# Kernel tuning notes

Hardware: AMD Instinct MI355X
Metric: run time of the kernel (lower is better)

The kernel has to match this reference:

```python
import jax, jax.numpy as jnp
import numpy as np

B, S, D = 2, 2048, 1024
H, HD = 16, 64

def setup_inputs() -> dict:
    key = jax.random.key(0)
    k1, k2, k3, k4 = jax.random.split(key, 4)
    inputs = jax.random.normal(k1, (B, S, D), dtype=jnp.float32)
    scale = 1.0 / np.sqrt(D)
    Wq = jax.random.normal(k2, (D, H * HD), dtype=jnp.float32) * scale
    Wk = jax.random.normal(k3, (D, H * HD), dtype=jnp.float32) * scale
    Wv = jax.random.normal(k4, (D, H * HD), dtype=jnp.float32) * scale
    return {"inputs": inputs, "Wq": Wq, "Wk": Wk, "Wv": Wv}

def _split_heads(x):
    # [B,S,H*HD] -> [B,H,S,HD]; tf.split along last axis == reshape then transpose
    b, s, _ = x.shape
    return x.reshape(b, s, H, HD).transpose(0, 2, 1, 3)

def reference(inputs, Wq, Wk, Wv):
    q = _split_heads(inputs @ Wq)  # [B,H,S,HD]
    k = _split_heads(inputs @ Wk)
    v = _split_heads(inputs @ Wv)
    scores = jnp.einsum("bhsd,bhtd->bhst", q, k) / jnp.sqrt(jnp.float32(HD))
    attn = jax.nn.softmax(scores, axis=-1)  # [B,H,S,S]
    out = jnp.einsum("bhst,bhtd->bhsd", attn, v)  # [B,H,S,HD]
    # concat heads back: [B,S,H*HD]
    return out.transpose(0, 2, 1, 3).reshape(inputs.shape[0], inputs.shape[1], H * HD)
```

## Files before the change

### kernel.cpp

```cpp
#include <hip/hip_runtime.h>
#include <hip/hip_fp16.h>

typedef __attribute__((ext_vector_type(8))) short short8;
typedef __attribute__((ext_vector_type(4))) float f32x4;
typedef __attribute__((ext_vector_type(16))) float f32x16;

#define B_  2
#define S_  2048
#define D_  1024
#define H_  16
#define HD_ 64
#define M_  (B_*S_)
#define N_  (H_*HD_)
#define HSZ ((size_t)B_*H_*S_*HD_)
#define BHS_ (B_*H_*S_)

#define QSCALE 0.18033688011112042f
#define M0 8.0f

__device__ __forceinline__ unsigned short f2bf(float f) {
  unsigned int u = __float_as_uint(f);
  u += 0x7fffu + ((u >> 16) & 1u);
  return (unsigned short)(u >> 16);
}

__device__ __forceinline__ unsigned int cvt_pk_bf16(float lo, float hi) {
  unsigned int r;
  asm("v_cvt_pk_bf16_f32 %0, %1, %2" : "=v"(r) : "v"(lo), "v"(hi));
  return r;
}

__device__ __forceinline__ float exp2_fast(float x) {
  float r;
  asm("v_exp_f32 %0, %1" : "=v"(r) : "v"(x));
  return r;
}

__device__ __forceinline__ void gll16(const void* g, void* l) {
  __builtin_amdgcn_global_load_lds(
      (const __attribute__((address_space(1))) void*)g,
      (__attribute__((address_space(3))) void*)l, 16, 0, 0);
}

__global__ __launch_bounds__(256) void cvt_all_kernel(const float* __restrict__ x,
                                                      const float* __restrict__ w0,
                                                      const float* __restrict__ w1,
                                                      const float* __restrict__ w2,
                                                      unsigned short* __restrict__ xb,
                                                      unsigned short* __restrict__ wt) {
  __shared__ float tile[32][33];
  int bid = blockIdx.x;
  if (bid < 4096) {
    int i = bid * 256 + threadIdx.x;
    float4 v = reinterpret_cast<const float4*>(x)[i];
    ushort4 o;
    o.x = f2bf(v.x); o.y = f2bf(v.y); o.z = f2bf(v.z); o.w = f2bf(v.w);
    reinterpret_cast<ushort4*>(xb)[i] = o;
    return;
  }
  int wid = bid - 4096;
  int z = wid >> 10, rem = wid & 1023;
  int nbase = (rem & 31) * 32, kbase = (rem >> 5) * 32;
  int tx = threadIdx.x & 31, ty = threadIdx.x >> 5;
  const float* w = z == 0 ? w0 : (z == 1 ? w1 : w2);
  unsigned short* o = wt + (size_t)z * D_ * N_;
#pragma unroll
  for (int i = 0; i < 4; i++)
    tile[ty + i*8][tx] = w[(size_t)(kbase + ty + i*8) * N_ + nbase + tx];
  __syncthreads();
#pragma unroll
  for (int i = 0; i < 4; i++)
    o[(size_t)(nbase + ty + i*8) * D_ + kbase + tx] = f2bf(tile[tx][ty + i*8]);
}

__global__ __launch_bounds__(256) void qkv_gemm_kernel(const unsigned short* __restrict__ xbp,
                                                       const unsigned short* __restrict__ wt,
                                                       unsigned short* __restrict__ qkv) {
  __shared__ __align__(16) unsigned short As[2][128 * 64];
  __shared__ __align__(16) unsigned short Bs[2][128 * 64];
  int hid = blockIdx.x;
  int wq = (hid & 7) * 96 + (hid >> 3);
  int z = wq >> 8, gy = (wq >> 3) & 31, gx = wq & 7;
  const unsigned short* w = wt + (size_t)z * D_ * N_;
  unsigned short* out = qkv + (size_t)z * HSZ;
  int lane = threadIdx.x & 63, wave = threadIdx.x >> 6;
  int lr = lane & 15, lk = lane >> 4;
  int mblk = gy * 128, nblk = gx * 128;
  int wm = (wave >> 1) * 64, wn = (wave & 1) * 64;

  int srow0 = wave * 32 + (lane >> 3);
  int scol = lane & 7;
  f32x4 acc[4][4] = {};

#define STAGE_G(b, kk) do {                                                      \
    _Pragma("unroll")                                                            \
    for (int it = 0; it < 4; it++) {                                             \
      int row = srow0 + it * 8;                                                  \
      int ce = (scol ^ (row & 7)) * 8;                                           \
      gll16(xbp + (size_t)(mblk + row) * D_ + (kk) + ce,                         \
            (void*)(As[b] + (size_t)(wave * 4 + it) * 512));                     \
      gll16(w   + (size_t)(nblk + row) * D_ + (kk) + ce,                         \
            (void*)(Bs[b] + (size_t)(wave * 4 + it) * 512));                     \
    }                                                                            \
  } while (0)

  STAGE_G(0, 0);

  for (int kt = 0; kt < 16; kt++) {
    int bufg = kt & 1;
    __syncthreads();
    if (kt < 15) STAGE_G(bufg ^ 1, (kt + 1) * 64);

    short8 a[2][4], b[2][4];
#pragma unroll
    for (int i = 0; i < 4; i++) {
      int row = wm + i * 16 + lr;
      const char* rp = (const char*)As[bufg] + row * 128;
#pragma unroll
      for (int ks = 0; ks < 2; ks++)
        a[ks][i] = *reinterpret_cast<const short8*>(rp + ((((ks*4 + lk) ^ (row & 7))) << 4));
    }
#pragma unroll
    for (int j = 0; j < 4; j++) {
      int row = wn + j * 16 + lr;
      const char* rp = (const char*)Bs[bufg] + row * 128;
#pragma unroll
      for (int ks = 0; ks < 2; ks++)
        b[ks][j] = *reinterpret_cast<const short8*>(rp + ((((ks*4 + lk) ^ (row & 7))) << 4));
    }
    if (z == 2) {
#pragma unroll
      for (int ks = 0; ks < 2; ks++)
#pragma unroll
        for (int i = 0; i < 4; i++)
#pragma unroll
          for (int j = 0; j < 4; j++)
            acc[i][j] = __builtin_amdgcn_mfma_f32_16x16x32_bf16(a[ks][i], b[ks][j], acc[i][j], 0, 0, 0);
    } else {
#pragma unroll
      for (int ks = 0; ks < 2; ks++)
#pragma unroll
        for (int i = 0; i < 4; i++)
#pragma unroll
          for (int j = 0; j < 4; j++)
            acc[i][j] = __builtin_amdgcn_mfma_f32_16x16x32_bf16(b[ks][j], a[ks][i], acc[i][j], 0, 0, 0);
    }
  }
#undef STAGE_G

  if (z == 2) {
#pragma unroll
    for (int i = 0; i < 4; i++) {
      int m0 = mblk + wm + i*16 + lk*4;
      int bb = m0 >> 11, s0 = m0 & (S_-1);
#pragma unroll
      for (int j = 0; j < 4; j++) {
        int n = nblk + wn + j*16 + lr;
        int h = n >> 6, d = n & (HD_-1);
        ushort4 pk;
        pk.x = f2bf(acc[i][j][0]); pk.y = f2bf(acc[i][j][1]);
        pk.z = f2bf(acc[i][j][2]); pk.w = f2bf(acc[i][j][3]);
        *reinterpret_cast<ushort4*>(out + ((size_t)(bb*H_ + h)*HD_ + d)*S_ + s0) = pk;
      }
    }
  } else {
    float qs = (z == 0) ? QSCALE : 1.0f;
#pragma unroll
    for (int i = 0; i < 4; i++) {
      int m = mblk + wm + i*16 + lr;
      int bb = m >> 11, s = m & (S_-1);
      unsigned short* ob = out + (size_t)bb*H_*S_*HD_ + (size_t)s*HD_;
#pragma unroll
      for (int j = 0; j < 4; j++) {
        int n0 = nblk + wn + j*16 + lk*4;
        int h = n0 >> 6, d = n0 & (HD_-1);
        ushort4 pk;
        pk.x = f2bf(acc[i][j][0]*qs); pk.y = f2bf(acc[i][j][1]*qs);
        pk.z = f2bf(acc[i][j][2]*qs); pk.w = f2bf(acc[i][j][3]*qs);
        *reinterpret_cast<ushort4*>(ob + (size_t)h*S_*HD_ + d) = pk;
      }
    }
  }
}

__global__ __launch_bounds__(256, 2) void attn_kernel(const unsigned short* __restrict__ qkv,
                                                      __half* __restrict__ Opart,
                                                      float* __restrict__ L) {
  int hid = blockIdx.x;
  int wrk = (hid & 7) * 64 + (hid >> 3);
  int bh = wrk >> 4, qt2 = (wrk >> 1) & 7, half = wrk & 1;

  const unsigned short* Q  = qkv +            (size_t)bh * S_ * HD_;
  const unsigned short* K  = qkv + HSZ   +    (size_t)bh * S_ * HD_;
  const unsigned short* Vt = qkv + 2*HSZ +    (size_t)bh * HD_ * S_;
  int lane = threadIdx.x & 63, wave = threadIdx.x >> 6;
  int ql = lane & 31, hi = lane >> 5;
  int qbase = qt2 * 256 + wave * 64;
  int tid = threadIdx.x;
  int kv0 = half * (S_/2);

  __shared__ __align__(16) unsigned short Ks[4][64 * 64];
  __shared__ __align__(16) unsigned short Vs[4][64 * 64];

#define STAGE(b, kc) do {                                                        \
    _Pragma("unroll")                                                            \
    for (int it = 0; it < 2; it++) {                                             \
      int ci = it * 256 + tid;                                                   \
      int rr = ci >> 3, cc = ci & 7;                                             \
      int ce = (cc ^ (rr & 7) ^ ((rr >> 3) & 7)) * 8;                            \
      gll16(K  + (size_t)((kc) + rr) * HD_ + ce, (void*)(Ks[b] + (size_t)ci*8)); \
      gll16(Vt + (size_t)rr * S_ + (kc) + ce,    (void*)(Vs[b] + (size_t)ci*8)); \
    }                                                                            \
  } while (0)

  short8 qf[2][4];
#pragma unroll
  for (int qt = 0; qt < 2; qt++)
#pragma unroll
    for (int ds = 0; ds < 4; ds++)
      qf[qt][ds] = *reinterpret_cast<const short8*>(
          Q + (size_t)(qbase + qt*32 + ql) * HD_ + ds*16 + hi*8);

  f32x16 oacc[2][2] = {};
  float lsum0 = 0.f, lsum1 = 0.f;

  STAGE(0, kv0);
  STAGE(1, kv0 + 64);

#pragma unroll 4
  for (int kt = 0; kt < 16; kt++) {
    int buf = kt & 3;
    if ((kt & 1) == 0) {
      __syncthreads();
      if (kt < 14) {
        STAGE((kt + 2) & 3, kv0 + (kt + 2) * 64);
        STAGE((kt + 3) & 3, kv0 + (kt + 3) * 64);
      }
    }

    short8 kf[2][4];
#pragma unroll
    for (int kh = 0; kh < 2; kh++) {
      int row = kh*32 + ql;
      const char* rp = (const char*)Ks[buf] + row * 128;
      int sw = (row & 7) ^ ((row >> 3) & 7);
#pragma unroll
      for (int ds = 0; ds < 4; ds++)
        kf[kh][ds] = *reinterpret_cast<const short8*>(rp + (((ds*2 + hi) ^ sw) << 4));
    }
    f32x16 s0[2], s1[2];
#pragma unroll
    for (int kh = 0; kh < 2; kh++)
#pragma unroll
      for (int r = 0; r < 16; r++) { s0[kh][r] = -M0; s1[kh][r] = -M0; }
    __builtin_amdgcn_s_setprio(1);
#pragma unroll
    for (int kh = 0; kh < 2; kh++)
#pragma unroll
      for (int ds = 0; ds < 4; ds++) {
        s0[kh] = __builtin_amdgcn_mfma_f32_32x32x16_bf16(kf[kh][ds], qf[0][ds], s0[kh], 0, 0, 0);
        s1[kh] = __builtin_amdgcn_mfma_f32_32x32x16_bf16(kf[kh][ds], qf[1][ds], s1[kh], 0, 0, 0);
      }
    __builtin_amdgcn_s_setprio(0);

#pragma unroll
    for (int kh = 0; kh < 2; kh++)
#pragma unroll
      for (int r = 0; r < 16; r++) {
        s0[kh][r] = exp2_fast(s0[kh][r]);
        s1[kh][r] = exp2_fast(s1[kh][r]);
      }
    {
      float ts[8];
#pragma unroll
      for (int r = 0; r < 8; r++)
        ts[r] = (s0[0][r] + s0[0][r+8]) + (s0[1][r] + s0[1][r+8]);
#pragma unroll
      for (int st = 4; st > 0; st >>= 1)
#pragma unroll
        for (int r = 0; r < st; r++) ts[r] += ts[r + st];
      lsum0 += ts[0] + __shfl_xor(ts[0], 32);
    }
    {
      float ts[8];
#pragma unroll
      for (int r = 0; r < 8; r++)
        ts[r] = (s1[0][r] + s1[0][r+8]) + (s1[1][r] + s1[1][r+8]);
#pragma unroll
      for (int st = 4; st > 0; st >>= 1)
#pragma unroll
        for (int r = 0; r < st; r++) ts[r] += ts[r + st];
      lsum1 += ts[0] + __shfl_xor(ts[0], 32);
    }

    short8 vf[4][2];
#pragma unroll
    for (int ks = 0; ks < 4; ks++) {
      int o = (ks & 1) * 8;
      int kh = ks >> 1;
      unsigned int w0 = cvt_pk_bf16(s0[kh][o+0], s0[kh][o+1]);
      unsigned int w1 = cvt_pk_bf16(s0[kh][o+2], s0[kh][o+3]);
      unsigned int w2 = cvt_pk_bf16(s0[kh][o+4], s0[kh][o+5]);
      unsigned int w3 = cvt_pk_bf16(s0[kh][o+6], s0[kh][o+7]);
      asm("v_permlane32_swap_b32 %0, %1" : "+v"(w0), "+v"(w2));
      asm("v_permlane32_swap_b32 %0, %1" : "+v"(w1), "+v"(w3));
      union { unsigned int u[4]; short8 v; } pf;
      pf.u[0] = w0; pf.u[1] = w1; pf.u[2] = w2; pf.u[3] = w3;
      __builtin_amdgcn_s_setprio(1);
#pragma unroll
      for (int dh = 0; dh < 2; dh++) {
        int row = dh*32 + ql;
        int sw = (row & 7) ^ ((row >> 3) & 7);
        vf[ks][dh] = *reinterpret_cast<const short8*>(
            (const char*)Vs[buf] + row * 128 + (((ks*2 + hi) ^ sw) << 4));
        oacc[0][dh] = __builtin_amdgcn_mfma_f32_32x32x16_bf16(vf[ks][dh], pf.v, oacc[0][dh], 0, 0, 0);
      }
      __builtin_amdgcn_s_setprio(0);
    }
#pragma unroll
    for (int ks = 0; ks < 4; ks++) {
      int o = (ks & 1) * 8;
      int kh = ks >> 1;
      unsigned int w0 = cvt_pk_bf16(s1[kh][o+0], s1[kh][o+1]);
      unsigned int w1 = cvt_pk_bf16(s1[kh][o+2], s1[kh][o+3]);
      unsigned int w2 = cvt_pk_bf16(s1[kh][o+4], s1[kh][o+5]);
      unsigned int w3 = cvt_pk_bf16(s1[kh][o+6], s1[kh][o+7]);
      asm("v_permlane32_swap_b32 %0, %1" : "+v"(w0), "+v"(w2));
      asm("v_permlane32_swap_b32 %0, %1" : "+v"(w1), "+v"(w3));
      union { unsigned int u[4]; short8 v; } pf;
      pf.u[0] = w0; pf.u[1] = w1; pf.u[2] = w2; pf.u[3] = w3;
      __builtin_amdgcn_s_setprio(1);
#pragma unroll
      for (int dh = 0; dh < 2; dh++)
        oacc[1][dh] = __builtin_amdgcn_mfma_f32_32x32x16_bf16(vf[ks][dh], pf.v, oacc[1][dh], 0, 0, 0);
      __builtin_amdgcn_s_setprio(0);
    }
  }

#pragma unroll
  for (int qt = 0; qt < 2; qt++) {
    int s = qbase + qt*32 + ql;
    size_t prow = (size_t)half * BHS_ + (size_t)bh * S_ + s;
    __half* orow = Opart + prow * HD_;
#pragma unroll
    for (int dh = 0; dh < 2; dh++)
#pragma unroll
      for (int a = 0; a < 4; a++) {
        union { __half2 h[2]; uint2 u; } pk;
        pk.h[0] = __float22half2_rn(make_float2(oacc[qt][dh][a*4+0], oacc[qt][dh][a*4+1]));
        pk.h[1] = __float22half2_rn(make_float2(oacc[qt][dh][a*4+2], oacc[qt][dh][a*4+3]));
        *reinterpret_cast<uint2*>(orow + dh*32 + 8*a + 4*hi) = pk.u;
      }
    if (hi == 0) L[prow] = (qt == 0) ? lsum0 : lsum1;
  }
#undef STAGE
}

__global__ __launch_bounds__(256) void combine_kernel(const __half* __restrict__ Opart,
                                                      const float* __restrict__ L,
                                                      float* __restrict__ out) {
  int idx = blockIdx.x * 256 + threadIdx.x;
  int row = idx >> 3;
  int dc = (idx & 7) * 8;
  float inv = 1.0f / (L[row] + L[BHS_ + row]);
  const __half2* p0 = reinterpret_cast<const __half2*>(Opart + (size_t)row * HD_ + dc);
  const __half2* p1 = reinterpret_cast<const __half2*>(Opart + ((size_t)BHS_ + row) * HD_ + dc);
  float r[8];
#pragma unroll
  for (int i = 0; i < 4; i++) {
    float2 a = __half22float2(p0[i]);
    float2 b = __half22float2(p1[i]);
    r[2*i+0] = (a.x + b.x) * inv;
    r[2*i+1] = (a.y + b.y) * inv;
  }
  int bh = row >> 11, s = row & (S_-1);
  int b = bh >> 4, h = bh & (H_-1);
  float* po = out + ((size_t)b * S_ + s) * N_ + h * HD_ + dc;
  float4 v0; v0.x = r[0]; v0.y = r[1]; v0.z = r[2]; v0.w = r[3];
  float4 v1; v1.x = r[4]; v1.y = r[5]; v1.z = r[6]; v1.w = r[7];
  *reinterpret_cast<float4*>(po)     = v0;
  *reinterpret_cast<float4*>(po + 4) = v1;
}

extern "C" void kernel_launch(void* const* d_in, const int* in_sizes, int n_in,
                              void* d_out, int out_size, void* d_ws, size_t ws_size,
                              hipStream_t stream) {
  const float* X  = (const float*)d_in[0];
  const float* Wq = (const float*)d_in[1];
  const float* Wk = (const float*)d_in[2];
  const float* Wv = (const float*)d_in[3];
  float* out = (float*)d_out;

  unsigned short* Xb  = (unsigned short*)d_ws;
  unsigned short* Wt  = Xb + (size_t)M_ * D_;
  unsigned short* QKV = Wt + (size_t)3 * D_ * N_;
  __half* Opart = (__half*)(QKV + 3 * HSZ);
  float* L    = (float*)(Opart + (size_t)2 * BHS_ * HD_);

  cvt_all_kernel<<<4096 + 3072, 256, 0, stream>>>(X, Wq, Wk, Wv, Xb, Wt);
  qkv_gemm_kernel<<<768, 256, 0, stream>>>(Xb, Wt, QKV);
  attn_kernel<<<(S_/256) * (B_*H_) * 2, 256, 0, stream>>>(QKV, Opart, L);
  combine_kernel<<<(BHS_*8)/256, 256, 0, stream>>>(Opart, L, out);
}
```

Baseline: 107.6 us.

## Triple-buffer QKV GEMM with K=32 stages and explicit vmcnt waits

Restructures the QKV projection GEMM main loop from a double-buffered K=64 pipeline into a triple-buffered K=32 pipeline with two stages of prefetch in flight. It uses a partial s_waitcnt vmcnt plus a raw barrier instead of __syncthreads, and sets launch bounds to 3 blocks per CU. LDS per block falls, which may raise occupancy, and a new XOR swizzle fits the 64-byte rows. In exchange it doubles the number of barriers per tile, and the hand-counted vmcnt must match the issued loads exactly to stay correct.

```diff
diff --git a/kernel.cpp b/kernel.cpp
--- a/kernel.cpp
+++ b/kernel.cpp
@@ -73,80 +73,87 @@
     o[(size_t)(nbase + ty + i*8) * D_ + kbase + tx] = f2bf(tile[tx][ty + i*8]);
 }
 
-__global__ __launch_bounds__(256) void qkv_gemm_kernel(const unsigned short* __restrict__ xbp,
-                                                       const unsigned short* __restrict__ wt,
-                                                       unsigned short* __restrict__ qkv) {
-  __shared__ __align__(16) unsigned short As[2][128 * 64];
-  __shared__ __align__(16) unsigned short Bs[2][128 * 64];
+__global__ __launch_bounds__(256, 3) void qkv_gemm_kernel(const unsigned short* __restrict__ xbp,
+                                                          const unsigned short* __restrict__ wt,
+                                                          unsigned short* __restrict__ qkv) {
+  __shared__ __align__(16) unsigned short As[3][128 * 32];
+  __shared__ __align__(16) unsigned short Bs[3][128 * 32];
   int hid = blockIdx.x;
   int wq = (hid & 7) * 96 + (hid >> 3);
-  int z = wq >> 8, gy = (wq >> 3) & 31, gx = wq & 7;
+  int z = wq >> 8, rem = wq & 255, gy = rem >> 3, gx = rem & 7;
   const unsigned short* w = wt + (size_t)z * D_ * N_;
   unsigned short* out = qkv + (size_t)z * HSZ;
   int lane = threadIdx.x & 63, wave = threadIdx.x >> 6;
   int lr = lane & 15, lk = lane >> 4;
   int mblk = gy * 128, nblk = gx * 128;
   int wm = (wave >> 1) * 64, wn = (wave & 1) * 64;
-
-  int srow0 = wave * 32 + (lane >> 3);
-  int scol = lane & 7;
+  int tid = threadIdx.x;
+
   f32x4 acc[4][4] = {};
 
 #define STAGE_G(b, kk) do {                                                      \
     _Pragma("unroll")                                                            \
-    for (int it = 0; it < 4; it++) {                                             \
-      int row = srow0 + it * 8;                                                  \
-      int ce = (scol ^ (row & 7)) * 8;                                           \
+    for (int it = 0; it < 2; it++) {                                             \
+      int ci = it * 256 + tid;                                                   \
+      int row = ci >> 2, c = ci & 3;                                             \
+      int ce = (c ^ (row & 3) ^ ((row >> 2) & 3)) * 8;                           \
       gll16(xbp + (size_t)(mblk + row) * D_ + (kk) + ce,                         \
-            (void*)(As[b] + (size_t)(wave * 4 + it) * 512));                     \
+            (void*)(As[b] + (size_t)ci * 8));                                    \
       gll16(w   + (size_t)(nblk + row) * D_ + (kk) + ce,                         \
-            (void*)(Bs[b] + (size_t)(wave * 4 + it) * 512));                     \
+            (void*)(Bs[b] + (size_t)ci * 8));                                    \
     }                                                                            \
   } while (0)
 
+#define COMPUTE_G(cb) do {                                                       \
+    short8 a[4], b[4];                                                           \
+    _Pragma("unroll")                                                            \
+    for (int i = 0; i < 4; i++) {                                                \
+      int row = wm + i * 16 + lr;                                                \
+      int sw = (row & 3) ^ ((row >> 2) & 3);                                     \
+      a[i] = *reinterpret_cast<const short8*>(                                   \
+          (const char*)As[cb] + row * 64 + ((lk ^ sw) << 4));                    \
+    }                                                                            \
+    _Pragma("unroll")                                                            \
+    for (int j = 0; j < 4; j++) {                                                \
+      int row = wn + j * 16 + lr;                                                \
+      int sw = (row & 3) ^ ((row >> 2) & 3);                                     \
+      b[j] = *reinterpret_cast<const short8*>(                                   \
+          (const char*)Bs[cb] + row * 64 + ((lk ^ sw) << 4));                    \
+    }                                                                            \
+    if (z == 2) {                                                                \
+      _Pragma("unroll")                                                          \
+      for (int i = 0; i < 4; i++)                                                \
+        _Pragma("unroll")                                                        \
+        for (int j = 0; j < 4; j++)                                              \
+          acc[i][j] = __builtin_amdgcn_mfma_f32_16x16x32_bf16(a[i], b[j], acc[i][j], 0, 0, 0); \
+    } else {                                                                     \
+      _Pragma("unroll")                                                          \
+      for (int i = 0; i < 4; i++)                                                \
+        _Pragma("unroll")                                                        \
+        for (int j = 0; j < 4; j++)                                              \
+          acc[i][j] = __builtin_amdgcn_mfma_f32_16x16x32_bf16(b[j], a[i], acc[i][j], 0, 0, 0); \
+    }                                                                            \
+  } while (0)
+
   STAGE_G(0, 0);
-
-  for (int kt = 0; kt < 16; kt++) {
-    int bufg = kt & 1;
-    __syncthreads();
-    if (kt < 15) STAGE_G(bufg ^ 1, (kt + 1) * 64);
-
-    short8 a[2][4], b[2][4];
-#pragma unroll
-    for (int i = 0; i < 4; i++) {
-      int row = wm + i * 16 + lr;
-      const char* rp = (const char*)As[bufg] + row * 128;
-#pragma unroll
-      for (int ks = 0; ks < 2; ks++)
-        a[ks][i] = *reinterpret_cast<const short8*>(rp + ((((ks*4 + lk) ^ (row & 7))) << 4));
-    }
-#pragma unroll
-    for (int j = 0; j < 4; j++) {
-      int row = wn + j * 16 + lr;
-      const char* rp = (const char*)Bs[bufg] + row * 128;
-#pragma unroll
-      for (int ks = 0; ks < 2; ks++)
-        b[ks][j] = *reinterpret_cast<const short8*>(rp + ((((ks*4 + lk) ^ (row & 7))) << 4));
-    }
-    if (z == 2) {
-#pragma unroll
-      for (int ks = 0; ks < 2; ks++)
-#pragma unroll
-        for (int i = 0; i < 4; i++)
-#pragma unroll
-          for (int j = 0; j < 4; j++)
-            acc[i][j] = __builtin_amdgcn_mfma_f32_16x16x32_bf16(a[ks][i], b[ks][j], acc[i][j], 0, 0, 0);
-    } else {
-#pragma unroll
-      for (int ks = 0; ks < 2; ks++)
-#pragma unroll
-        for (int i = 0; i < 4; i++)
-#pragma unroll
-          for (int j = 0; j < 4; j++)
-            acc[i][j] = __builtin_amdgcn_mfma_f32_16x16x32_bf16(b[ks][j], a[ks][i], acc[i][j], 0, 0, 0);
-    }
-  }
+  STAGE_G(1, 32);
+
+  int cur = 0, stg = 2;
+  for (int kt = 0; kt < 31; kt++) {
+    asm volatile("s_waitcnt vmcnt(4)" ::: "memory");
+    __builtin_amdgcn_s_barrier();
+    __builtin_amdgcn_sched_barrier(0);
+    if (kt < 30) STAGE_G(stg, (kt + 2) * 32);
+    COMPUTE_G(cur);
+    cur = (cur == 2) ? 0 : cur + 1;
+    stg = (stg == 2) ? 0 : stg + 1;
+  }
+  asm volatile("s_waitcnt vmcnt(0)" ::: "memory");
+  __builtin_amdgcn_s_barrier();
+  __builtin_amdgcn_sched_barrier(0);
+  COMPUTE_G(cur);
 #undef STAGE_G
+#undef COMPUTE_G
 
   if (z == 2) {
 #pragma unroll
```

Measured after the change: 121.2 us. +12.6%, slower.

## Deepen K staging ring and prefetch next-tile K fragments into registers

Applied to the files above, without the earlier changes.

Splits K and V staging so that K tiles are prefetched one tile further ahead, using a 5-deep LDS ring for K. The K fragments for the next tile are now loaded into registers during the current iteration, and all V fragment LDS reads are hoisted ahead of the softmax exp work. The goal is to hide LDS and global latency behind the exp and MFMA work. In exchange it uses more LDS and more registers, and it fully unrolls the loop, which could reduce occupancy or cause spills.

```diff
diff --git a/kernel.cpp b/kernel.cpp
--- a/kernel.cpp
+++ b/kernel.cpp
@@ -199,19 +199,38 @@
   int tid = threadIdx.x;
   int kv0 = half * (S_/2);
 
-  __shared__ __align__(16) unsigned short Ks[4][64 * 64];
+  __shared__ __align__(16) unsigned short Ks[5][64 * 64];
   __shared__ __align__(16) unsigned short Vs[4][64 * 64];
 
-#define STAGE(b, kc) do {                                                        \
+#define STAGE_K(b, kc) do {                                                      \
     _Pragma("unroll")                                                            \
     for (int it = 0; it < 2; it++) {                                             \
       int ci = it * 256 + tid;                                                   \
       int rr = ci >> 3, cc = ci & 7;                                             \
       int ce = (cc ^ (rr & 7) ^ ((rr >> 3) & 7)) * 8;                            \
-      gll16(K  + (size_t)((kc) + rr) * HD_ + ce, (void*)(Ks[b] + (size_t)ci*8)); \
+      gll16(K + (size_t)((kc) + rr) * HD_ + ce, (void*)(Ks[b] + (size_t)ci*8));  \
+    }                                                                            \
+  } while (0)
+#define STAGE_V(b, kc) do {                                                      \
+    _Pragma("unroll")                                                            \
+    for (int it = 0; it < 2; it++) {                                             \
+      int ci = it * 256 + tid;                                                   \
+      int rr = ci >> 3, cc = ci & 7;                                             \
+      int ce = (cc ^ (rr & 7) ^ ((rr >> 3) & 7)) * 8;                            \
       gll16(Vt + (size_t)rr * S_ + (kc) + ce,    (void*)(Vs[b] + (size_t)ci*8)); \
     }                                                                            \
   } while (0)
+#define LOAD_KF(kb) do {                                                         \
+    _Pragma("unroll")                                                            \
+    for (int kh = 0; kh < 2; kh++) {                                             \
+      int row = kh*32 + ql;                                                      \
+      const char* rp = (const char*)Ks[kb] + row * 128;                          \
+      int sw = (row & 7) ^ ((row >> 3) & 7);                                     \
+      _Pragma("unroll")                                                          \
+      for (int ds = 0; ds < 4; ds++)                                             \
+        kf[kh][ds] = *reinterpret_cast<const short8*>(rp + (((ds*2 + hi) ^ sw) << 4)); \
+    }                                                                            \
+  } while (0)
 
   short8 qf[2][4];
 #pragma unroll
@@ -224,30 +243,23 @@
   f32x16 oacc[2][2] = {};
   float lsum0 = 0.f, lsum1 = 0.f;
 
-  STAGE(0, kv0);
-  STAGE(1, kv0 + 64);
-
-#pragma unroll 4
+  STAGE_K(0, kv0); STAGE_K(1, kv0 + 64); STAGE_K(2, kv0 + 128);
+  STAGE_V(0, kv0); STAGE_V(1, kv0 + 64);
+  __syncthreads();
+
+  short8 kf[2][4];
+  LOAD_KF(0);
+
+#pragma unroll
   for (int kt = 0; kt < 16; kt++) {
-    int buf = kt & 3;
     if ((kt & 1) == 0) {
       __syncthreads();
-      if (kt < 14) {
-        STAGE((kt + 2) & 3, kv0 + (kt + 2) * 64);
-        STAGE((kt + 3) & 3, kv0 + (kt + 3) * 64);
-      }
-    }
-
-    short8 kf[2][4];
-#pragma unroll
-    for (int kh = 0; kh < 2; kh++) {
-      int row = kh*32 + ql;
-      const char* rp = (const char*)Ks[buf] + row * 128;
-      int sw = (row & 7) ^ ((row >> 3) & 7);
-#pragma unroll
-      for (int ds = 0; ds < 4; ds++)
-        kf[kh][ds] = *reinterpret_cast<const short8*>(rp + (((ds*2 + hi) ^ sw) << 4));
-    }
+      if (kt + 3 < 16) STAGE_K((kt + 3) % 5, kv0 + (kt + 3) * 64);
+      if (kt + 4 < 16) STAGE_K((kt + 4) % 5, kv0 + (kt + 4) * 64);
+      if (kt + 2 < 16) STAGE_V((kt + 2) & 3, kv0 + (kt + 2) * 64);
+      if (kt + 3 < 16) STAGE_V((kt + 3) & 3, kv0 + (kt + 3) * 64);
+    }
+
     f32x16 s0[2], s1[2];
 #pragma unroll
     for (int kh = 0; kh < 2; kh++)
@@ -263,6 +275,19 @@
       }
     __builtin_amdgcn_s_setprio(0);
 
+    short8 vf[4][2];
+#pragma unroll
+    for (int ks = 0; ks < 4; ks++)
+#pragma unroll
+      for (int dh = 0; dh < 2; dh++) {
+        int row = dh*32 + ql;
+        int sw = (row & 7) ^ ((row >> 3) & 7);
+        vf[ks][dh] = *reinterpret_cast<const short8*>(
+            (const char*)Vs[kt & 3] + row * 128 + (((ks*2 + hi) ^ sw) << 4));
+      }
+
+    if (kt < 15) LOAD_KF((kt + 1) % 5);
+
 #pragma unroll
     for (int kh = 0; kh < 2; kh++)
 #pragma unroll
@@ -293,7 +318,6 @@
       lsum1 += ts[0] + __shfl_xor(ts[0], 32);
     }
 
-    short8 vf[4][2];
 #pragma unroll
     for (int ks = 0; ks < 4; ks++) {
       int o = (ks & 1) * 8;
@@ -308,13 +332,8 @@
       pf.u[0] = w0; pf.u[1] = w1; pf.u[2] = w2; pf.u[3] = w3;
       __builtin_amdgcn_s_setprio(1);
 #pragma unroll
-      for (int dh = 0; dh < 2; dh++) {
-        int row = dh*32 + ql;
-        int sw = (row & 7) ^ ((row >> 3) & 7);
-        vf[ks][dh] = *reinterpret_cast<const short8*>(
-            (const char*)Vs[buf] + row * 128 + (((ks*2 + hi) ^ sw) << 4));
+      for (int dh = 0; dh < 2; dh++)
         oacc[0][dh] = __builtin_amdgcn_mfma_f32_32x32x16_bf16(vf[ks][dh], pf.v, oacc[0][dh], 0, 0, 0);
-      }
       __builtin_amdgcn_s_setprio(0);
     }
 #pragma unroll
@@ -353,7 +372,9 @@
       }
     if (hi == 0) L[prow] = (qt == 0) ? lsum0 : lsum1;
   }
-#undef STAGE
+#undef STAGE_K
+#undef STAGE_V
+#undef LOAD_KF
 }
 
 __global__ __launch_bounds__(256) void combine_kernel(const __half* __restrict__ Opart,
```

After: 162.5 us. 1.51x slower.

## Drop split-KV attention and combine kernel, normalize output in attention epilogue

Applied to the files above, without the earlier changes.

Each attention block now processes the full KV range (32 tiles) instead of half, so the partial-output buffer, the L sums and the separate combine kernel go away. The epilogue divides by the row sum and writes fp32 output straight into the final [B,S,H*HD] layout. This removes one launch and the round trip of fp16 partials through global memory. In exchange the grid halves to 256 blocks, which may underfill the GPU's compute units and lengthen each block's serial loop.

```diff
diff --git a/kernel.cpp b/kernel.cpp
--- a/kernel.cpp
+++ b/kernel.cpp
@@ -13,7 +13,6 @@
 #define M_  (B_*S_)
 #define N_  (H_*HD_)
 #define HSZ ((size_t)B_*H_*S_*HD_)
-#define BHS_ (B_*H_*S_)
 
 #define QSCALE 0.18033688011112042f
 #define M0 8.0f
@@ -184,11 +183,10 @@
 }
 
 __global__ __launch_bounds__(256, 2) void attn_kernel(const unsigned short* __restrict__ qkv,
-                                                      __half* __restrict__ Opart,
-                                                      float* __restrict__ L) {
+                                                      float* __restrict__ out) {
   int hid = blockIdx.x;
-  int wrk = (hid & 7) * 64 + (hid >> 3);
-  int bh = wrk >> 4, qt2 = (wrk >> 1) & 7, half = wrk & 1;
+  int wrk = (hid & 7) * 32 + (hid >> 3);
+  int bh = wrk >> 3, qt2 = wrk & 7;
 
   const unsigned short* Q  = qkv +            (size_t)bh * S_ * HD_;
   const unsigned short* K  = qkv + HSZ   +    (size_t)bh * S_ * HD_;
@@ -197,7 +195,6 @@
   int ql = lane & 31, hi = lane >> 5;
   int qbase = qt2 * 256 + wave * 64;
   int tid = threadIdx.x;
-  int kv0 = half * (S_/2);
 
   __shared__ __align__(16) unsigned short Ks[4][64 * 64];
   __shared__ __align__(16) unsigned short Vs[4][64 * 64];
@@ -224,17 +221,17 @@
   f32x16 oacc[2][2] = {};
   float lsum0 = 0.f, lsum1 = 0.f;
 
-  STAGE(0, kv0);
-  STAGE(1, kv0 + 64);
+  STAGE(0, 0);
+  STAGE(1, 64);
 
 #pragma unroll 4
-  for (int kt = 0; kt < 16; kt++) {
+  for (int kt = 0; kt < 32; kt++) {
     int buf = kt & 3;
     if ((kt & 1) == 0) {
       __syncthreads();
-      if (kt < 14) {
-        STAGE((kt + 2) & 3, kv0 + (kt + 2) * 64);
-        STAGE((kt + 3) & 3, kv0 + (kt + 3) * 64);
+      if (kt < 30) {
+        STAGE((kt + 2) & 3, (kt + 2) * 64);
+        STAGE((kt + 3) & 3, (kt + 3) * 64);
       }
     }
 
@@ -337,49 +334,23 @@
     }
   }
 
+  int b0 = bh >> 4, h = bh & (H_-1);
 #pragma unroll
   for (int qt = 0; qt < 2; qt++) {
+    float inv = 1.0f / ((qt == 0) ? lsum0 : lsum1);
     int s = qbase + qt*32 + ql;
-    size_t prow = (size_t)half * BHS_ + (size_t)bh * S_ + s;
-    __half* orow = Opart + prow * HD_;
+    float* orow = out + ((size_t)b0 * S_ + s) * N_ + h * HD_;
 #pragma unroll
     for (int dh = 0; dh < 2; dh++)
 #pragma unroll
       for (int a = 0; a < 4; a++) {
-        union { __half2 h[2]; uint2 u; } pk;
-        pk.h[0] = __float22half2_rn(make_float2(oacc[qt][dh][a*4+0], oacc[qt][dh][a*4+1]));
-        pk.h[1] = __float22half2_rn(make_float2(oacc[qt][dh][a*4+2], oacc[qt][dh][a*4+3]));
-        *reinterpret_cast<uint2*>(orow + dh*32 + 8*a + 4*hi) = pk.u;
-      }
-    if (hi == 0) L[prow] = (qt == 0) ? lsum0 : lsum1;
+        float4 vv;
+        vv.x = oacc[qt][dh][a*4+0] * inv; vv.y = oacc[qt][dh][a*4+1] * inv;
+        vv.z = oacc[qt][dh][a*4+2] * inv; vv.w = oacc[qt][dh][a*4+3] * inv;
+        *reinterpret_cast<float4*>(orow + dh*32 + 8*a + 4*hi) = vv;
+      }
   }
 #undef STAGE
-}
-
-__global__ __launch_bounds__(256) void combine_kernel(const __half* __restrict__ Opart,
-                                                      const float* __restrict__ L,
-                                                      float* __restrict__ out) {
-  int idx = blockIdx.x * 256 + threadIdx.x;
-  int row = idx >> 3;
-  int dc = (idx & 7) * 8;
-  float inv = 1.0f / (L[row] + L[BHS_ + row]);
-  const __half2* p0 = reinterpret_cast<const __half2*>(Opart + (size_t)row * HD_ + dc);
-  const __half2* p1 = reinterpret_cast<const __half2*>(Opart + ((size_t)BHS_ + row) * HD_ + dc);
-  float r[8];
-#pragma unroll
-  for (int i = 0; i < 4; i++) {
-    float2 a = __half22float2(p0[i]);
-    float2 b = __half22float2(p1[i]);
-    r[2*i+0] = (a.x + b.x) * inv;
-    r[2*i+1] = (a.y + b.y) * inv;
-  }
-  int bh = row >> 11, s = row & (S_-1);
-  int b = bh >> 4, h = bh & (H_-1);
-  float* po = out + ((size_t)b * S_ + s) * N_ + h * HD_ + dc;
-  float4 v0; v0.x = r[0]; v0.y = r[1]; v0.z = r[2]; v0.w = r[3];
-  float4 v1; v1.x = r[4]; v1.y = r[5]; v1.z = r[6]; v1.w = r[7];
-  *reinterpret_cast<float4*>(po)     = v0;
-  *reinterpret_cast<float4*>(po + 4) = v1;
 }
 
 extern "C" void kernel_launch(void* const* d_in, const int* in_sizes, int n_in,
@@ -394,11 +365,8 @@
   unsigned short* Xb  = (unsigned short*)d_ws;
   unsigned short* Wt  = Xb + (size_t)M_ * D_;
   unsigned short* QKV = Wt + (size_t)3 * D_ * N_;
-  __half* Opart = (__half*)(QKV + 3 * HSZ);
-  float* L    = (float*)(Opart + (size_t)2 * BHS_ * HD_);
 
   cvt_all_kernel<<<4096 + 3072, 256, 0, stream>>>(X, Wq, Wk, Wv, Xb, Wt);
   qkv_gemm_kernel<<<768, 256, 0, stream>>>(Xb, Wt, QKV);
-  attn_kernel<<<(S_/256) * (B_*H_) * 2, 256, 0, stream>>>(QKV, Opart, L);
-  combine_kernel<<<(BHS_*8)/256, 256, 0, stream>>>(Opart, L, out);
-}
+  attn_kernel<<<(S_/256) * (B_*H_), 256, 0, stream>>>(QKV, out);
+}
```

New measurement: 117.1 us. 1.09x slower.
